# Kernel optimization log

Measured on AMD Instinct MI355X. Metric: run time of the kernel, lower is better.

## Reference

```python
import jax, jax.numpy as jnp
import numpy as np

B, T, N, H = 256, 128, 1024, 1024


def setup_inputs() -> dict:
    key = jax.random.key(0)
    ks = jax.random.split(key, 7)
    s = 0.05
    return {
        "input_data": jax.random.normal(ks[0], (B, T, N), jnp.float32),
        "W_ih": jax.random.normal(ks[1], (4 * H, N), jnp.float32) * s,
        "W_hh": jax.random.normal(ks[2], (4 * H, H), jnp.float32) * s,
        "b_ih": jax.random.normal(ks[3], (4 * H,), jnp.float32) * s,
        "b_hh": jax.random.normal(ks[4], (4 * H,), jnp.float32) * s,
        "attn_w": jax.random.normal(ks[5], (2 * H + T,), jnp.float32) * s,
        "attn_b": jax.random.normal(ks[6], (1,), jnp.float32) * s,
    }


def reference(input_data, W_ih, W_hh, b_ih, b_hh, attn_w, attn_b):
    # input_data: [B, T, N]; torch LSTM gate order i, f, g, o.
    Bsz, Tn, Nn = input_data.shape
    Hn = W_hh.shape[1]
    # Decompose the attn linear over the concat [h, c, x_hist]:
    # score = h @ w_h + c @ w_c + x_perm @ w_x + b  (exactly the original Linear)
    w_h, w_c, w_x = attn_w[:Hn], attn_w[Hn:2 * Hn], attn_w[2 * Hn:]
    x_perm = jnp.transpose(input_data, (0, 2, 1))            # [B, N, T]
    score_x = x_perm @ w_x + attn_b[0]                        # [B, N], constant over t

    def step(carry, x_t):
        h, c = carry                                          # [B, H] each
        score = (h @ w_h + c @ w_c)[:, None] + score_x        # [B, N]
        a = jax.nn.softmax(score, axis=1)                     # [B, N]
        w_in = a * x_t                                        # weighted input [B, N]
        gates = w_in @ W_ih.T + b_ih + h @ W_hh.T + b_hh      # [B, 4H]
        i, f, g, o = jnp.split(gates, 4, axis=1)
        c_new = jax.nn.sigmoid(f) * c + jax.nn.sigmoid(i) * jnp.tanh(g)
        h_new = jax.nn.sigmoid(o) * jnp.tanh(c_new)
        return (h_new, c_new), (w_in, h_new)

    h0 = jnp.zeros((Bsz, Hn), input_data.dtype)
    c0 = jnp.zeros((Bsz, Hn), input_data.dtype)
    xs = jnp.transpose(input_data, (1, 0, 2))                 # [T, B, N]
    _, (iw, ie) = jax.lax.scan(step, (h0, c0), xs)
    input_weighted = jnp.transpose(iw, (1, 0, 2))             # [B, T, N]
    input_encoded = jnp.transpose(ie, (1, 0, 2))              # [B, T, H]
    return input_weighted, input_encoded
```

## Files before the change

### kernel.cpp

```cpp
#include <hip/hip_runtime.h>
#include <hip/hip_bf16.h>

#define BB 256
#define TT 128
#define NN 1024
#define HH 1024
#define G4 4096

typedef __attribute__((ext_vector_type(4))) float f32x4;
typedef __attribute__((ext_vector_type(8))) short bf16x8;

__device__ __forceinline__ unsigned short f2bf(float f) {
    unsigned int u = __builtin_bit_cast(unsigned int, f);
    u += 0x7FFFu + ((u >> 16) & 1u);
    return (unsigned short)(u >> 16);
}
__device__ __forceinline__ float bf2f(unsigned short s) {
    unsigned int u = ((unsigned int)s) << 16;
    return __builtin_bit_cast(float, u);
}

__global__ __launch_bounds__(512) void k_attn(
    const float* __restrict__ x, const float* __restrict__ attn_w,
    const float* __restrict__ attn_b, float* __restrict__ out0,
    unsigned short* __restrict__ win_bf)
{
    const int b = blockIdx.x;
    const int tid = threadIdx.x;
    const float* xb = x + (size_t)b * (TT * NN);
    const float* wx = attn_w + 2 * HH;

    float s0 = 0.f, s1 = 0.f;
    for (int t = 0; t < TT; ++t) {
        float2 v = *(const float2*)(xb + (size_t)t * NN + tid * 2);
        float w = wx[t];
        s0 += v.x * w; s1 += v.y * w;
    }
    float ab = attn_b[0];
    s0 += ab; s1 += ab;

    __shared__ float red[8];
    const int wv = tid >> 6, ln = tid & 63;
    float m = fmaxf(s0, s1);
#pragma unroll
    for (int off = 32; off > 0; off >>= 1) m = fmaxf(m, __shfl_xor(m, off));
    if (ln == 0) red[wv] = m;
    __syncthreads();
    m = red[0];
#pragma unroll
    for (int i = 1; i < 8; ++i) m = fmaxf(m, red[i]);

    float e0 = expf(s0 - m), e1 = expf(s1 - m);
    float sum = e0 + e1;
#pragma unroll
    for (int off = 32; off > 0; off >>= 1) sum += __shfl_xor(sum, off);
    __syncthreads();
    if (ln == 0) red[wv] = sum;
    __syncthreads();
    sum = 0.f;
#pragma unroll
    for (int i = 0; i < 8; ++i) sum += red[i];
    const float inv = 1.0f / sum;
    const float a0 = e0 * inv, a1 = e1 * inv;

    float* o = out0 + (size_t)b * (TT * NN);
    unsigned short* wb = win_bf + (size_t)b * (TT * NN);
    for (int t = 0; t < TT; ++t) {
        float2 v = *(const float2*)(xb + (size_t)t * NN + tid * 2);
        float2 w; w.x = a0 * v.x; w.y = a1 * v.y;
        *(float2*)(o + (size_t)t * NN + tid * 2) = w;
        unsigned int pk = (unsigned int)f2bf(w.x) | ((unsigned int)f2bf(w.y) << 16);
        *(unsigned int*)(wb + (size_t)t * NN + tid * 2) = pk;
    }
}

__global__ __launch_bounds__(256) void k_prep_w(
    const float* __restrict__ Wih, const float* __restrict__ Whh,
    const float* __restrict__ bih, const float* __restrict__ bhh,
    unsigned short* __restrict__ WihP, unsigned short* __restrict__ WhhP,
    float* __restrict__ biasP)
{
    const int p = blockIdx.x;
    const int j = p >> 2, g = p & 3;
    const int r = g * HH + j;
    const int tid = threadIdx.x;
    {
        float4 v = *(const float4*)(Wih + (size_t)r * NN + tid * 4);
        ushort4 o;
        o.x = f2bf(v.x); o.y = f2bf(v.y); o.z = f2bf(v.z); o.w = f2bf(v.w);
        *(ushort4*)(WihP + (size_t)p * NN + tid * 4) = o;
    }
    {
        float4 v = *(const float4*)(Whh + (size_t)r * HH + tid * 4);
        ushort4 o;
        o.x = f2bf(v.x); o.y = f2bf(v.y); o.z = f2bf(v.z); o.w = f2bf(v.w);
        *(ushort4*)(WhhP + (size_t)p * HH + tid * 4) = o;
    }
    if (tid == 0) biasP[p] = bih[r] + bhh[r];
}

__global__ __launch_bounds__(256) void k_gemm_xp(
    const unsigned short* __restrict__ A,
    const unsigned short* __restrict__ Bm,
    unsigned short* __restrict__ C)
{
    __shared__ unsigned short lA[128 * 32];
    __shared__ unsigned short lB[128 * 32];

    const int bid = blockIdx.x;
    const int cpx = gridDim.x >> 3;
    const int swz = (bid & 7) * cpx + (bid >> 3);
    const int NTN = G4 / 128;
    const int tm = swz / NTN, tn = swz % NTN;

    const int tid = threadIdx.x;
    const int wv = tid >> 6, ln = tid & 63;
    const int wr = wv >> 1, wc = wv & 1;

    f32x4 acc[4][4] = {};

    const unsigned short* Ag = A + (size_t)tm * 128 * NN;
    const unsigned short* Bg = Bm + (size_t)tn * 128 * NN;
    const int srow = ln >> 2;
    const int sseg = ln & 3;

    for (int k0 = 0; k0 < NN; k0 += 32) {
        __syncthreads();
#pragma unroll
        for (int q = 0; q < 2; ++q) {
            const int row = wv * 32 + q * 16 + srow;
            __builtin_amdgcn_global_load_lds(
                (const __attribute__((address_space(1))) void*)(Ag + (size_t)row * NN + k0 + sseg * 8),
                (__attribute__((address_space(3))) void*)(&lA[(wv * 32 + q * 16) * 32]),
                16, 0, 0);
            __builtin_amdgcn_global_load_lds(
                (const __attribute__((address_space(1))) void*)(Bg + (size_t)row * NN + k0 + sseg * 8),
                (__attribute__((address_space(3))) void*)(&lB[(wv * 32 + q * 16) * 32]),
                16, 0, 0);
        }
        __syncthreads();

        const int rlo = ln & 15, khi = ln >> 4;
        bf16x8 af[4], bfr[4];
#pragma unroll
        for (int m = 0; m < 4; ++m)
            af[m] = *(const bf16x8*)&lA[(wr * 64 + m * 16 + rlo) * 32 + khi * 8];
#pragma unroll
        for (int n = 0; n < 4; ++n)
            bfr[n] = *(const bf16x8*)&lB[(wc * 64 + n * 16 + rlo) * 32 + khi * 8];
#pragma unroll
        for (int m = 0; m < 4; ++m)
#pragma unroll
            for (int n = 0; n < 4; ++n)
                acc[m][n] = __builtin_amdgcn_mfma_f32_16x16x32_bf16(af[m], bfr[n], acc[m][n], 0, 0, 0);
    }

    const int rlo = ln & 15, rhi = ln >> 4;
#pragma unroll
    for (int m = 0; m < 4; ++m)
#pragma unroll
        for (int n = 0; n < 4; ++n)
#pragma unroll
            for (int j = 0; j < 4; ++j) {
                const int row = tm * 128 + wr * 64 + m * 16 + rhi * 4 + j;
                const int col = tn * 128 + wc * 64 + n * 16 + rlo;
                C[(size_t)row * G4 + col] = f2bf(acc[m][n][j]);
            }
}

__global__ __launch_bounds__(512) void k_step3(
    const int t,
    const unsigned short* __restrict__ hbf,
    const unsigned short* __restrict__ WhhP,
    const unsigned short* __restrict__ Xp,
    const float* __restrict__ biasP,
    float* __restrict__ cbuf,
    unsigned short* __restrict__ hbf_out,
    float* __restrict__ out1)
{
    __shared__ unsigned short lA[3][64 * 128];
    __shared__ unsigned short lB[3][64 * 128];
    __shared__ unsigned short lXp[64 * 64];

    const int bid = blockIdx.x;
    const int ti = bid >> 6, tj = bid & 63;
    const int tid = threadIdx.x;
    const int wv = tid >> 6, ln = tid & 63;
    const int wr = wv >> 1, wc = wv & 1;
    const int rlo = ln & 15, khi = ln >> 4;

    {
        const size_t bg = (size_t)(ti * 64 + wv * 8 + (ln >> 3));
        __builtin_amdgcn_global_load_lds(
            (const __attribute__((address_space(1))) void*)((const char*)Xp + ((bg * TT + t) << 13) + tj * 128 + (ln & 7) * 16),
            (__attribute__((address_space(3))) void*)((char*)lXp + wv * 1024),
            16, 0, 0);
    }

    const char* Ab = (const char*)hbf + (size_t)(ti * 64) * 2048;
    const char* Bb = (const char*)WhhP + (size_t)(tj * 64) * 2048;

#define STAGE(buf_, c_) do { \
    _Pragma("unroll") \
    for (int q_ = 0; q_ < 2; ++q_) { \
        const int r_ = q_ * 32 + wv * 4 + (ln >> 4); \
        const int so_ = (((ln & 15) ^ (r_ & 7)) << 4); \
        __builtin_amdgcn_global_load_lds( \
            (const __attribute__((address_space(1))) void*)(Ab + (size_t)r_ * 2048 + (c_) * 256 + so_), \
            (__attribute__((address_space(3))) void*)((char*)&lA[buf_][0] + q_ * 8192 + wv * 1024), \
            16, 0, 0); \
        __builtin_amdgcn_global_load_lds( \
            (const __attribute__((address_space(1))) void*)(Bb + (size_t)r_ * 2048 + (c_) * 256 + so_), \
            (__attribute__((address_space(3))) void*)((char*)&lB[buf_][0] + q_ * 8192 + wv * 1024), \
            16, 0, 0); \
    } } while (0)

    STAGE(0, 0);
    STAGE(1, 1);
    STAGE(2, 2);

    float4 bias4[2];
#pragma unroll
    for (int n = 0; n < 2; ++n)
        bias4[n] = *(const float4*)&biasP[(tj * 16 + wc * 8 + n * 4 + ((ln & 15) >> 2)) * 4];

    f32x4 acc[2] = {};

#pragma unroll
    for (int c = 0; c < 8; ++c) {
        const int buf = c % 3;
        if (c < 6)       { asm volatile("s_waitcnt vmcnt(8)" ::: "memory"); }
        else if (c == 6) { asm volatile("s_waitcnt vmcnt(4)" ::: "memory"); }
        else             { asm volatile("s_waitcnt vmcnt(0)" ::: "memory"); }
        __builtin_amdgcn_s_barrier();

        bf16x8 af[4], bfr[4][2];
#pragma unroll
        for (int kk = 0; kk < 4; ++kk) {
            {
                const int row = wr * 16 + rlo;
                const int off = (kk * 64 + khi * 16) ^ ((row & 7) << 4);
                af[kk] = *(const bf16x8*)((const char*)&lA[buf][0] + row * 256 + off);
            }
#pragma unroll
            for (int n = 0; n < 2; ++n) {
                const int row = wc * 32 + n * 16 + rlo;
                const int off = (kk * 64 + khi * 16) ^ ((row & 7) << 4);
                bfr[kk][n] = *(const bf16x8*)((const char*)&lB[buf][0] + row * 256 + off);
            }
        }
        asm volatile("s_waitcnt lgkmcnt(0)" ::: "memory");
        __builtin_amdgcn_sched_barrier(0);
        __builtin_amdgcn_s_barrier();
        if (c < 5) STAGE((c + 3) % 3, c + 3);
#pragma unroll
        for (int kk = 0; kk < 4; ++kk)
#pragma unroll
            for (int n = 0; n < 2; ++n)
                acc[n] = __builtin_amdgcn_mfma_f32_16x16x32_bf16(af[kk], bfr[kk][n], acc[n], 0, 0, 0);
    }
#undef STAGE

#pragma unroll
    for (int n = 0; n < 2; ++n) {
        f32x4 v = acc[n], u, w;
#pragma unroll
        for (int k = 0; k < 4; ++k) {
            float s = __shfl_xor(v[k ^ 1], 1);
            u[k] = ((k & 1) == (ln & 1)) ? v[k] : s;
        }
#pragma unroll
        for (int k = 0; k < 4; ++k) {
            float s = __shfl_xor(u[k ^ 2], 2);
            w[k] = (((k >> 1) & 1) == ((ln >> 1) & 1)) ? u[k] : s;
        }
        const int r_loc = wr * 16 + ((ln >> 4) << 2) + (ln & 3);
        const int u_loc = wc * 8 + n * 4 + ((ln & 15) >> 2);
        const ushort4 xp4 = *(const ushort4*)((const char*)lXp + r_loc * 128 + u_loc * 8);
        const float gi = w[0] + bf2f(xp4.x) + bias4[n].x;
        const float gf = w[1] + bf2f(xp4.y) + bias4[n].y;
        const float gg = w[2] + bf2f(xp4.z) + bias4[n].z;
        const float go = w[3] + bf2f(xp4.w) + bias4[n].w;
        const float i_ = 1.f / (1.f + expf(-gi));
        const float f_ = 1.f / (1.f + expf(-gf));
        const float g_ = tanhf(gg);
        const float o_ = 1.f / (1.f + expf(-go));
        const int bg = ti * 64 + r_loc;
        const int ug = tj * 16 + u_loc;
        const float cprev = cbuf[(size_t)bg * HH + ug];
        const float cc = f_ * cprev + i_ * g_;
        cbuf[(size_t)bg * HH + ug] = cc;
        const float h_ = o_ * tanhf(cc);
        out1[(size_t)bg * (TT * HH) + (size_t)t * HH + ug] = h_;
        hbf_out[(size_t)bg * HH + ug] = f2bf(h_);
    }
}

__global__ __launch_bounds__(256) void k_zero(float4* __restrict__ p)
{
    p[blockIdx.x * 256 + threadIdx.x] = make_float4(0.f, 0.f, 0.f, 0.f);
}

extern "C" void kernel_launch(void* const* d_in, const int* in_sizes, int n_in,
                              void* d_out, int out_size, void* d_ws, size_t ws_size,
                              hipStream_t stream)
{
    const float* x      = (const float*)d_in[0];
    const float* Wih    = (const float*)d_in[1];
    const float* Whh    = (const float*)d_in[2];
    const float* bih    = (const float*)d_in[3];
    const float* bhh    = (const float*)d_in[4];
    const float* attn_w = (const float*)d_in[5];
    const float* attn_b = (const float*)d_in[6];

    float* out0 = (float*)d_out;
    float* out1 = (float*)d_out + (size_t)BB * TT * NN;

    char* w = (char*)d_ws;
    unsigned short* WihP  = (unsigned short*)(w);
    unsigned short* WhhP  = (unsigned short*)(w + 8388608);
    float*          biasP = (float*)(w + 16777216);
    unsigned short* winbf = (unsigned short*)(w + 16793600);
    unsigned short* Xp    = (unsigned short*)(w + 83902464);
    unsigned short* hbf0  = (unsigned short*)(w + 352337920);
    unsigned short* hbf1  = (unsigned short*)(w + 352862208);
    float*          cbuf  = (float*)(w + 353386496);

    k_attn<<<BB, 512, 0, stream>>>(x, attn_w, attn_b, out0, winbf);
    k_prep_w<<<G4, 256, 0, stream>>>(Wih, Whh, bih, bhh, WihP, WhhP, biasP);
    k_gemm_xp<<<(BB * TT / 128) * (G4 / 128), 256, 0, stream>>>(winbf, WihP, Xp);
    k_zero<<<512, 256, 0, stream>>>((float4*)hbf0);

    for (int t = 0; t < TT; ++t) {
        const unsigned short* hin = (t & 1) ? hbf1 : hbf0;
        unsigned short* hout      = (t & 1) ? hbf0 : hbf1;
        k_step3<<<256, 512, 0, stream>>>(t, hin, WhhP, Xp, biasP, cbuf, hout, out1);
    }
}
```

Before: 1.717 ms.

## Replace per-timestep launches with persistent cooperative LSTM recurrence kernel

Adds a persistent cooperative kernel that runs all 128 timesteps in one launch. Each block keeps its slice of W_hh resident in LDS for the whole sequence and keeps the cell state in registers. Blocks sharing a batch tile synchronise through per-tile atomic counters in global memory instead of kernel boundaries. This removes per-step launch overhead and repeated W_hh reloads, at the cost of spin-wait latency, reliance on every block being co-resident, and reuse of the cbuf region as counters. The old per-step launch loop is kept as a fallback if the cooperative launch fails.

Result: slower. 2.731 ms (+59.0%).

```diff
diff --git a/kernel.cpp b/kernel.cpp
--- a/kernel.cpp
+++ b/kernel.cpp
@@ -166,6 +166,154 @@
                 const int col = tn * 128 + wc * 64 + n * 16 + rlo;
                 C[(size_t)row * G4 + col] = f2bf(acc[m][n][j]);
             }
+}
+
+__global__ __launch_bounds__(512, 1) void k_recur2(
+    const unsigned short* __restrict__ WhhP,
+    const unsigned short* __restrict__ Xp,
+    const float* __restrict__ biasP,
+    unsigned short* __restrict__ h0,
+    unsigned short* __restrict__ h1,
+    unsigned int* __restrict__ ctr,
+    float* __restrict__ out1)
+{
+    __shared__ unsigned short lB[64 * 1024];
+    __shared__ unsigned short lA[3][64 * 64];
+
+    const int bid = blockIdx.x;
+    const int ti = bid >> 6, tj = bid & 63;
+    const int tid = threadIdx.x;
+    const int wv = tid >> 6, ln = tid & 63;
+    const int wr = wv >> 1, wc = wv & 1;
+    const int rlo = ln & 15, khi = ln >> 4;
+
+    {
+        const char* base = (const char*)WhhP + (size_t)(tj * 64) * 2048;
+#pragma unroll
+        for (int q = 0; q < 16; ++q) {
+            const int i = wv * 16 + q;
+            const int r = i >> 1, half = i & 1;
+            const int lbo = (half * 1024 + ln * 16) ^ ((r & 7) << 4);
+            __builtin_amdgcn_global_load_lds(
+                (const __attribute__((address_space(1))) void*)(base + (size_t)r * 2048 + lbo),
+                (__attribute__((address_space(3))) void*)((char*)lB + i * 1024),
+                16, 0, 0);
+        }
+    }
+
+    float4 bias4[2];
+#pragma unroll
+    for (int n = 0; n < 2; ++n)
+        bias4[n] = *(const float4*)&biasP[(tj * 16 + wc * 8 + n * 4 + ((ln & 15) >> 2)) * 4];
+
+    const int r_loc = wr * 16 + ((ln >> 4) << 2) + (ln & 3);
+    const int u_loc0 = wc * 8 + ((ln & 15) >> 2);
+    const int bg = ti * 64 + r_loc;
+    unsigned int* myctr = &ctr[ti * 64];
+
+    float c_reg[2] = {0.f, 0.f};
+
+#define STAGE_H(buf_, c_) do { \
+    const int r_ = wv * 8 + (ln >> 3); \
+    const int so_ = ((ln & 7) << 4) ^ ((r_ & 7) << 4); \
+    __builtin_amdgcn_global_load_lds( \
+        (const __attribute__((address_space(1))) void*)(Ab + (size_t)r_ * 2048 + (c_) * 128 + so_), \
+        (__attribute__((address_space(3))) void*)((char*)&lA[buf_][0] + wv * 1024), \
+        16, 0, 0); \
+} while (0)
+
+    for (int t = 0; t < TT; ++t) {
+        const unsigned short* hR = (t & 1) ? h1 : h0;
+        unsigned short* hW = (t & 1) ? h0 : h1;
+
+        ushort4 xp4[2];
+#pragma unroll
+        for (int n = 0; n < 2; ++n)
+            xp4[n] = *(const ushort4*)((const char*)Xp +
+                        ((size_t)bg * TT + t) * 8192 + tj * 128 + (u_loc0 + n * 4) * 8);
+
+        f32x4 acc[2] = {};
+
+        if (t > 0) {
+            if (tid == 0) {
+                const unsigned int want = 64u * (unsigned int)t;
+                while (__hip_atomic_load(myctr, __ATOMIC_RELAXED, __HIP_MEMORY_SCOPE_AGENT) < want)
+                    __builtin_amdgcn_s_sleep(2);
+                (void)__hip_atomic_load(myctr, __ATOMIC_ACQUIRE, __HIP_MEMORY_SCOPE_AGENT);
+            }
+            __syncthreads();
+
+            const char* Ab = (const char*)hR + (size_t)(ti * 64) * 2048;
+            STAGE_H(0, 0);
+            STAGE_H(1, 1);
+#pragma unroll
+            for (int c = 0; c < 16; ++c) {
+                const int buf = c % 3;
+                if (c < 15) { asm volatile("s_waitcnt vmcnt(1)" ::: "memory"); }
+                else        { asm volatile("s_waitcnt vmcnt(0)" ::: "memory"); }
+                __builtin_amdgcn_s_barrier();
+                if (c < 14) STAGE_H((c + 2) % 3, c + 2);
+
+                bf16x8 af[2], bfr[2][2];
+#pragma unroll
+                for (int kk = 0; kk < 2; ++kk) {
+                    {
+                        const int row = wr * 16 + rlo;
+                        const int off = (kk * 64 + khi * 16) ^ ((row & 7) << 4);
+                        af[kk] = *(const bf16x8*)((const char*)&lA[buf][0] + row * 128 + off);
+                    }
+#pragma unroll
+                    for (int n = 0; n < 2; ++n) {
+                        const int row = wc * 32 + n * 16 + rlo;
+                        const int off = (c * 128 + kk * 64 + khi * 16) ^ ((row & 7) << 4);
+                        bfr[kk][n] = *(const bf16x8*)((const char*)lB + row * 2048 + off);
+                    }
+                }
+                asm volatile("s_waitcnt lgkmcnt(0)" ::: "memory");
+                __builtin_amdgcn_sched_barrier(0);
+#pragma unroll
+                for (int kk = 0; kk < 2; ++kk)
+#pragma unroll
+                    for (int n = 0; n < 2; ++n)
+                        acc[n] = __builtin_amdgcn_mfma_f32_16x16x32_bf16(af[kk], bfr[kk][n], acc[n], 0, 0, 0);
+            }
+        }
+
+#pragma unroll
+        for (int n = 0; n < 2; ++n) {
+            f32x4 v = acc[n], u, w;
+#pragma unroll
+            for (int k = 0; k < 4; ++k) {
+                float s = __shfl_xor(v[k ^ 1], 1);
+                u[k] = ((k & 1) == (ln & 1)) ? v[k] : s;
+            }
+#pragma unroll
+            for (int k = 0; k < 4; ++k) {
+                float s = __shfl_xor(u[k ^ 2], 2);
+                w[k] = (((k >> 1) & 1) == ((ln >> 1) & 1)) ? u[k] : s;
+            }
+            const float gi = w[0] + bf2f(xp4[n].x) + bias4[n].x;
+            const float gf = w[1] + bf2f(xp4[n].y) + bias4[n].y;
+            const float gg = w[2] + bf2f(xp4[n].z) + bias4[n].z;
+            const float go = w[3] + bf2f(xp4[n].w) + bias4[n].w;
+            const float i_ = 1.f / (1.f + expf(-gi));
+            const float f_ = 1.f / (1.f + expf(-gf));
+            const float g_ = tanhf(gg);
+            const float o_ = 1.f / (1.f + expf(-go));
+            const float cc = f_ * c_reg[n] + i_ * g_;
+            c_reg[n] = cc;
+            const float h_ = o_ * tanhf(cc);
+            const int ug = tj * 16 + u_loc0 + n * 4;
+            __builtin_nontemporal_store(h_, &out1[(size_t)bg * (TT * HH) + (size_t)t * HH + ug]);
+            hW[(size_t)bg * HH + ug] = f2bf(h_);
+        }
+
+        asm volatile("s_waitcnt vmcnt(0)" ::: "memory");
+        __syncthreads();
+        if (tid == 0)
+            __hip_atomic_fetch_add(myctr, 1u, __ATOMIC_RELEASE, __HIP_MEMORY_SCOPE_AGENT);
+    }
+#undef STAGE_H
 }
 
 __global__ __launch_bounds__(512) void k_step3(
@@ -331,9 +479,24 @@
     k_gemm_xp<<<(BB * TT / 128) * (G4 / 128), 256, 0, stream>>>(winbf, WihP, Xp);
     k_zero<<<512, 256, 0, stream>>>((float4*)hbf0);
 
-    for (int t = 0; t < TT; ++t) {
-        const unsigned short* hin = (t & 1) ? hbf1 : hbf0;
-        unsigned short* hout      = (t & 1) ? hbf0 : hbf1;
-        k_step3<<<256, 512, 0, stream>>>(t, hin, WhhP, Xp, biasP, cbuf, hout, out1);
-    }
-}
+    {
+        const unsigned short* WhhP_c = WhhP;
+        const unsigned short* Xp_c = Xp;
+        const float* biasP_c = biasP;
+        unsigned short* h0_c = hbf0;
+        unsigned short* h1_c = hbf1;
+        unsigned int* ctr_c = (unsigned int*)cbuf;
+        float* out1_c = out1;
+        void* args[] = { (void*)&WhhP_c, (void*)&Xp_c, (void*)&biasP_c,
+                         (void*)&h0_c, (void*)&h1_c, (void*)&ctr_c, (void*)&out1_c };
+        hipError_t err = hipLaunchCooperativeKernel((void*)k_recur2, dim3(256), dim3(512),
+                                                    args, 0, stream);
+        if (err != hipSuccess) {
+            for (int t = 0; t < TT; ++t) {
+                const unsigned short* hin = (t & 1) ? hbf1 : hbf0;
+                unsigned short* hout      = (t & 1) ? hbf0 : hbf1;
+                k_step3<<<256, 512, 0, stream>>>(t, hin, WhhP, Xp, biasP, cbuf, hout, out1);
+            }
+        }
+    }
+}
```

## Restructure LSTM step kernel: full-K LDS weight tile, direct-register h loads

Applied to the files above, without the earlier changes.

The per-step recurrent GEMM kernel is rewritten to stage the whole 64x1024 W_hh tile into LDS in two halves through registers, replacing the triple-buffered global_load_lds pipeline over K chunks. The h operand is now read straight from global memory into registers instead of through LDS. The Xp slice, previous cell state and bias are prefetched into registers at kernel start, which removes most per-chunk barriers. The cost is 128KB of LDS per block and heavy register use, with launch_bounds(512,2) added as an occupancy hint.

New measurement: 2.232 ms. +30.0%, slower.

```diff
diff --git a/kernel.cpp b/kernel.cpp
--- a/kernel.cpp
+++ b/kernel.cpp
@@ -168,7 +168,7 @@
             }
 }
 
-__global__ __launch_bounds__(512) void k_step3(
+__global__ __launch_bounds__(512, 2) void k_step4(
     const int t,
     const unsigned short* __restrict__ hbf,
     const unsigned short* __restrict__ WhhP,
@@ -178,9 +178,7 @@
     unsigned short* __restrict__ hbf_out,
     float* __restrict__ out1)
 {
-    __shared__ unsigned short lA[3][64 * 128];
-    __shared__ unsigned short lB[3][64 * 128];
-    __shared__ unsigned short lXp[64 * 64];
+    __shared__ unsigned short lB[64 * 1024];
 
     const int bid = blockIdx.x;
     const int ti = bid >> 6, tj = bid & 63;
@@ -188,78 +186,95 @@
     const int wv = tid >> 6, ln = tid & 63;
     const int wr = wv >> 1, wc = wv & 1;
     const int rlo = ln & 15, khi = ln >> 4;
-
-    {
-        const size_t bg = (size_t)(ti * 64 + wv * 8 + (ln >> 3));
-        __builtin_amdgcn_global_load_lds(
-            (const __attribute__((address_space(1))) void*)((const char*)Xp + ((bg * TT + t) << 13) + tj * 128 + (ln & 7) * 16),
-            (__attribute__((address_space(3))) void*)((char*)lXp + wv * 1024),
-            16, 0, 0);
-    }
+    const int khi16 = khi * 16;
 
     const char* Ab = (const char*)hbf + (size_t)(ti * 64) * 2048;
     const char* Bb = (const char*)WhhP + (size_t)(tj * 64) * 2048;
 
-#define STAGE(buf_, c_) do { \
-    _Pragma("unroll") \
-    for (int q_ = 0; q_ < 2; ++q_) { \
-        const int r_ = q_ * 32 + wv * 4 + (ln >> 4); \
-        const int so_ = (((ln & 15) ^ (r_ & 7)) << 4); \
-        __builtin_amdgcn_global_load_lds( \
-            (const __attribute__((address_space(1))) void*)(Ab + (size_t)r_ * 2048 + (c_) * 256 + so_), \
-            (__attribute__((address_space(3))) void*)((char*)&lA[buf_][0] + q_ * 8192 + wv * 1024), \
-            16, 0, 0); \
-        __builtin_amdgcn_global_load_lds( \
-            (const __attribute__((address_space(1))) void*)(Bb + (size_t)r_ * 2048 + (c_) * 256 + so_), \
-            (__attribute__((address_space(3))) void*)((char*)&lB[buf_][0] + q_ * 8192 + wv * 1024), \
-            16, 0, 0); \
-    } } while (0)
-
-    STAGE(0, 0);
-    STAGE(1, 1);
-    STAGE(2, 2);
-
+    const int r_loc = wr * 16 + ((ln >> 4) << 2) + (ln & 3);
+    const int u_loc0 = wc * 8 + ((ln & 15) >> 2);
+    const int bg = ti * 64 + r_loc;
+
+    ushort4 xp4[2];
+    float cp[2];
     float4 bias4[2];
 #pragma unroll
-    for (int n = 0; n < 2; ++n)
-        bias4[n] = *(const float4*)&biasP[(tj * 16 + wc * 8 + n * 4 + ((ln & 15) >> 2)) * 4];
+    for (int n = 0; n < 2; ++n) {
+        xp4[n] = *(const ushort4*)((const char*)Xp +
+                    ((size_t)bg * TT + t) * 8192 + tj * 128 + (u_loc0 + n * 4) * 8);
+        cp[n] = cbuf[(size_t)bg * HH + tj * 16 + u_loc0 + n * 4];
+        bias4[n] = *(const float4*)&biasP[(tj * 16 + u_loc0 + n * 4) * 4];
+    }
+
+    const int srow = tid >> 3;
+    const int sseg = tid & 7;
+    const int sswz = (srow & 7) << 4;
+
+    bf16x8 bh1[8];
+#pragma unroll
+    for (int j = 0; j < 8; ++j)
+        bh1[j] = *(const bf16x8*)(Bb + (size_t)srow * 2048 + (sseg + j * 8) * 16);
+
+    const char* abase = Ab + (size_t)(wr * 16 + rlo) * 2048 + khi16;
+#define LOADA(c) \
+    const bf16x8 a0_##c = *(const bf16x8*)(abase + (c) * 128); \
+    const bf16x8 a1_##c = *(const bf16x8*)(abase + (c) * 128 + 64);
+    LOADA(0) LOADA(1) LOADA(2) LOADA(3) LOADA(4) LOADA(5) LOADA(6) LOADA(7)
+
+    bf16x8 bh2[8];
+#pragma unroll
+    for (int j = 0; j < 8; ++j)
+        bh2[j] = *(const bf16x8*)(Bb + (size_t)srow * 2048 + 1024 + (sseg + j * 8) * 16);
+
+    char* lw = (char*)lB + (size_t)srow * 2048;
+#pragma unroll
+    for (int j = 0; j < 8; ++j)
+        *(bf16x8*)(lw + (((sseg + j * 8) * 16) ^ sswz)) = bh1[j];
+
+    asm volatile("s_waitcnt lgkmcnt(0)" ::: "memory");
+    __builtin_amdgcn_sched_barrier(0);
+    __builtin_amdgcn_s_barrier();
+
+    const int brow0 = wc * 32 + rlo;
+    const int bswz = (brow0 & 7) << 4;
+    const char* lb0 = (const char*)lB + (size_t)brow0 * 2048;
+    const char* lb1 = lb0 + 16 * 2048;
+    const int okk0 = khi16 ^ bswz;
+    const int okk1 = (64 + khi16) ^ bswz;
 
     f32x4 acc[2] = {};
 
-#pragma unroll
-    for (int c = 0; c < 8; ++c) {
-        const int buf = c % 3;
-        if (c < 6)       { asm volatile("s_waitcnt vmcnt(8)" ::: "memory"); }
-        else if (c == 6) { asm volatile("s_waitcnt vmcnt(4)" ::: "memory"); }
-        else             { asm volatile("s_waitcnt vmcnt(0)" ::: "memory"); }
-        __builtin_amdgcn_s_barrier();
-
-        bf16x8 af[4], bfr[4][2];
-#pragma unroll
-        for (int kk = 0; kk < 4; ++kk) {
-            {
-                const int row = wr * 16 + rlo;
-                const int off = (kk * 64 + khi * 16) ^ ((row & 7) << 4);
-                af[kk] = *(const bf16x8*)((const char*)&lA[buf][0] + row * 256 + off);
-            }
-#pragma unroll
-            for (int n = 0; n < 2; ++n) {
-                const int row = wc * 32 + n * 16 + rlo;
-                const int off = (kk * 64 + khi * 16) ^ ((row & 7) << 4);
-                bfr[kk][n] = *(const bf16x8*)((const char*)&lB[buf][0] + row * 256 + off);
-            }
-        }
-        asm volatile("s_waitcnt lgkmcnt(0)" ::: "memory");
-        __builtin_amdgcn_sched_barrier(0);
-        __builtin_amdgcn_s_barrier();
-        if (c < 5) STAGE((c + 3) % 3, c + 3);
-#pragma unroll
-        for (int kk = 0; kk < 4; ++kk)
-#pragma unroll
-            for (int n = 0; n < 2; ++n)
-                acc[n] = __builtin_amdgcn_mfma_f32_16x16x32_bf16(af[kk], bfr[kk][n], acc[n], 0, 0, 0);
-    }
-#undef STAGE
+#define CHUNK(c) do { \
+    const bf16x8 b00 = *(const bf16x8*)(lb0 + (c) * 128 + okk0); \
+    const bf16x8 b01 = *(const bf16x8*)(lb0 + (c) * 128 + okk1); \
+    const bf16x8 b10 = *(const bf16x8*)(lb1 + (c) * 128 + okk0); \
+    const bf16x8 b11 = *(const bf16x8*)(lb1 + (c) * 128 + okk1); \
+    acc[0] = __builtin_amdgcn_mfma_f32_16x16x32_bf16(a0_##c, b00, acc[0], 0, 0, 0); \
+    acc[1] = __builtin_amdgcn_mfma_f32_16x16x32_bf16(a0_##c, b10, acc[1], 0, 0, 0); \
+    acc[0] = __builtin_amdgcn_mfma_f32_16x16x32_bf16(a1_##c, b01, acc[0], 0, 0, 0); \
+    acc[1] = __builtin_amdgcn_mfma_f32_16x16x32_bf16(a1_##c, b11, acc[1], 0, 0, 0); \
+} while (0)
+
+    CHUNK(0); CHUNK(1); CHUNK(2);
+
+#pragma unroll
+    for (int j = 0; j < 8; ++j)
+        *(bf16x8*)(lw + 1024 + (((sseg + j * 8) * 16) ^ sswz)) = bh2[j];
+
+    CHUNK(3); CHUNK(4);
+    LOADA(8) LOADA(9) LOADA(10) LOADA(11)
+    CHUNK(5); CHUNK(6);
+    LOADA(12) LOADA(13) LOADA(14) LOADA(15)
+    CHUNK(7);
+
+    asm volatile("s_waitcnt lgkmcnt(0)" ::: "memory");
+    __builtin_amdgcn_sched_barrier(0);
+    __builtin_amdgcn_s_barrier();
+
+    CHUNK(8); CHUNK(9); CHUNK(10); CHUNK(11);
+    CHUNK(12); CHUNK(13); CHUNK(14); CHUNK(15);
+#undef CHUNK
+#undef LOADA
 
 #pragma unroll
     for (int n = 0; n < 2; ++n) {
@@ -274,23 +289,18 @@
             float s = __shfl_xor(u[k ^ 2], 2);
             w[k] = (((k >> 1) & 1) == ((ln >> 1) & 1)) ? u[k] : s;
         }
-        const int r_loc = wr * 16 + ((ln >> 4) << 2) + (ln & 3);
-        const int u_loc = wc * 8 + n * 4 + ((ln & 15) >> 2);
-        const ushort4 xp4 = *(const ushort4*)((const char*)lXp + r_loc * 128 + u_loc * 8);
-        const float gi = w[0] + bf2f(xp4.x) + bias4[n].x;
-        const float gf = w[1] + bf2f(xp4.y) + bias4[n].y;
-        const float gg = w[2] + bf2f(xp4.z) + bias4[n].z;
-        const float go = w[3] + bf2f(xp4.w) + bias4[n].w;
+        const float gi = w[0] + bf2f(xp4[n].x) + bias4[n].x;
+        const float gf = w[1] + bf2f(xp4[n].y) + bias4[n].y;
+        const float gg = w[2] + bf2f(xp4[n].z) + bias4[n].z;
+        const float go = w[3] + bf2f(xp4[n].w) + bias4[n].w;
         const float i_ = 1.f / (1.f + expf(-gi));
         const float f_ = 1.f / (1.f + expf(-gf));
         const float g_ = tanhf(gg);
         const float o_ = 1.f / (1.f + expf(-go));
-        const int bg = ti * 64 + r_loc;
-        const int ug = tj * 16 + u_loc;
-        const float cprev = cbuf[(size_t)bg * HH + ug];
-        const float cc = f_ * cprev + i_ * g_;
+        const float cc = f_ * cp[n] + i_ * g_;
+        const float h_ = o_ * tanhf(cc);
+        const int ug = tj * 16 + u_loc0 + n * 4;
         cbuf[(size_t)bg * HH + ug] = cc;
-        const float h_ = o_ * tanhf(cc);
         out1[(size_t)bg * (TT * HH) + (size_t)t * HH + ug] = h_;
         hbf_out[(size_t)bg * HH + ug] = f2bf(h_);
     }
@@ -334,6 +344,6 @@
     for (int t = 0; t < TT; ++t) {
         const unsigned short* hin = (t & 1) ? hbf1 : hbf0;
         unsigned short* hout      = (t & 1) ? hbf0 : hbf1;
-        k_step3<<<256, 512, 0, stream>>>(t, hin, WhhP, Xp, biasP, cbuf, hout, out1);
-    }
-}
+        k_step4<<<256, 512, 0, stream>>>(t, hin, WhhP, Xp, biasP, cbuf, hout, out1);
+    }
+}
```

## Rewrite input-projection GEMM with 256x256 tiles and triple-buffered async LDS pipeline

Applied to the files above, without the earlier changes.

Replaces the 128x128-tile input projection GEMM with a 512-thread kernel using 256x256 tiles, a 64-wide K chunk and a three-stage LDS ring filled by global_load_lds. Explicit vmcnt waits and barriers let the next loads overlap with the MFMA work, and s_setprio raises priority during the MFMA section. The aim is more reuse per loaded byte and hidden global latency in the big precompute GEMM. In exchange it uses much more LDS and registers, which limits occupancy to one block per CU, and it depends on hand-tuned waitcnt counts being correct.

Measured after the change: 1.832 ms. +6.7%, slower.

```diff
diff --git a/kernel.cpp b/kernel.cpp
--- a/kernel.cpp
+++ b/kernel.cpp
@@ -99,71 +99,85 @@
     if (tid == 0) biasP[p] = bih[r] + bhh[r];
 }
 
-__global__ __launch_bounds__(256) void k_gemm_xp(
+__global__ __launch_bounds__(512, 1) void k_gemm_xp2(
     const unsigned short* __restrict__ A,
     const unsigned short* __restrict__ Bm,
     unsigned short* __restrict__ C)
 {
-    __shared__ unsigned short lA[128 * 32];
-    __shared__ unsigned short lB[128 * 32];
+    __shared__ unsigned short lA[3][4][256][8];
+    __shared__ unsigned short lB[3][4][256][8];
 
     const int bid = blockIdx.x;
     const int cpx = gridDim.x >> 3;
     const int swz = (bid & 7) * cpx + (bid >> 3);
-    const int NTN = G4 / 128;
+    const int NTN = G4 / 256;
     const int tm = swz / NTN, tn = swz % NTN;
 
     const int tid = threadIdx.x;
     const int wv = tid >> 6, ln = tid & 63;
-    const int wr = wv >> 1, wc = wv & 1;
-
-    f32x4 acc[4][4] = {};
-
-    const unsigned short* Ag = A + (size_t)tm * 128 * NN;
-    const unsigned short* Bg = Bm + (size_t)tn * 128 * NN;
-    const int srow = ln >> 2;
-    const int sseg = ln & 3;
-
-    for (int k0 = 0; k0 < NN; k0 += 32) {
-        __syncthreads();
-#pragma unroll
-        for (int q = 0; q < 2; ++q) {
-            const int row = wv * 32 + q * 16 + srow;
-            __builtin_amdgcn_global_load_lds(
-                (const __attribute__((address_space(1))) void*)(Ag + (size_t)row * NN + k0 + sseg * 8),
-                (__attribute__((address_space(3))) void*)(&lA[(wv * 32 + q * 16) * 32]),
-                16, 0, 0);
-            __builtin_amdgcn_global_load_lds(
-                (const __attribute__((address_space(1))) void*)(Bg + (size_t)row * NN + k0 + sseg * 8),
-                (__attribute__((address_space(3))) void*)(&lB[(wv * 32 + q * 16) * 32]),
-                16, 0, 0);
-        }
-        __syncthreads();
-
-        const int rlo = ln & 15, khi = ln >> 4;
-        bf16x8 af[4], bfr[4];
-#pragma unroll
-        for (int m = 0; m < 4; ++m)
-            af[m] = *(const bf16x8*)&lA[(wr * 64 + m * 16 + rlo) * 32 + khi * 8];
+    const int wm = wv >> 2, wn = wv & 3;
+    const int rlo = ln & 15, khi = ln >> 4;
+
+    const char* Ag = (const char*)A + (size_t)(tm * 256) * 2048;
+    const char* Bg = (const char*)Bm + (size_t)(tn * 256) * 2048;
+
+#define STAGE(buf_, c_) do { \
+    _Pragma("unroll") \
+    for (int j_ = 0; j_ < 2; ++j_) { \
+        const int seg_ = (wv * 2 + j_) * 64 + ln; \
+        const int khi_ = seg_ >> 8, row_ = seg_ & 255; \
+        __builtin_amdgcn_global_load_lds( \
+            (const __attribute__((address_space(1))) void*)(Ag + (size_t)row_ * 2048 + (c_) * 64 + khi_ * 16), \
+            (__attribute__((address_space(3))) void*)((char*)&lA[buf_][0][0][0] + (wv * 2 + j_) * 1024), \
+            16, 0, 0); \
+        __builtin_amdgcn_global_load_lds( \
+            (const __attribute__((address_space(1))) void*)(Bg + (size_t)row_ * 2048 + (c_) * 64 + khi_ * 16), \
+            (__attribute__((address_space(3))) void*)((char*)&lB[buf_][0][0][0] + (wv * 2 + j_) * 1024), \
+            16, 0, 0); \
+    } } while (0)
+
+    STAGE(0, 0); STAGE(1, 1); STAGE(2, 2);
+
+    f32x4 acc[8][4] = {};
+
+    for (int c = 0; c < 32; ++c) {
+        const int buf = c % 3;
+        if (c < 30)       { asm volatile("s_waitcnt vmcnt(8)" ::: "memory"); }
+        else if (c == 30) { asm volatile("s_waitcnt vmcnt(4)" ::: "memory"); }
+        else              { asm volatile("s_waitcnt vmcnt(0)" ::: "memory"); }
+        __builtin_amdgcn_s_barrier();
+
+        bf16x8 af[8], bfr[4];
+#pragma unroll
+        for (int m = 0; m < 8; ++m)
+            af[m] = *(const bf16x8*)&lA[buf][khi][wm * 128 + m * 16 + rlo][0];
 #pragma unroll
         for (int n = 0; n < 4; ++n)
-            bfr[n] = *(const bf16x8*)&lB[(wc * 64 + n * 16 + rlo) * 32 + khi * 8];
-#pragma unroll
-        for (int m = 0; m < 4; ++m)
+            bfr[n] = *(const bf16x8*)&lB[buf][khi][wn * 64 + n * 16 + rlo][0];
+        asm volatile("s_waitcnt lgkmcnt(0)" ::: "memory");
+        __builtin_amdgcn_sched_barrier(0);
+        __builtin_amdgcn_s_barrier();
+        if (c < 29) STAGE(buf, c + 3);
+
+        __builtin_amdgcn_s_setprio(1);
+#pragma unroll
+        for (int m = 0; m < 8; ++m)
 #pragma unroll
             for (int n = 0; n < 4; ++n)
                 acc[m][n] = __builtin_amdgcn_mfma_f32_16x16x32_bf16(af[m], bfr[n], acc[m][n], 0, 0, 0);
-    }
-
-    const int rlo = ln & 15, rhi = ln >> 4;
-#pragma unroll
-    for (int m = 0; m < 4; ++m)
+        __builtin_amdgcn_s_setprio(0);
+    }
+#undef STAGE
+
+    const int rhi = ln >> 4;
+#pragma unroll
+    for (int m = 0; m < 8; ++m)
 #pragma unroll
         for (int n = 0; n < 4; ++n)
 #pragma unroll
             for (int j = 0; j < 4; ++j) {
-                const int row = tm * 128 + wr * 64 + m * 16 + rhi * 4 + j;
-                const int col = tn * 128 + wc * 64 + n * 16 + rlo;
+                const int row = tm * 256 + wm * 128 + m * 16 + rhi * 4 + j;
+                const int col = tn * 256 + wn * 64 + n * 16 + rlo;
                 C[(size_t)row * G4 + col] = f2bf(acc[m][n][j]);
             }
 }
@@ -328,7 +342,7 @@
 
     k_attn<<<BB, 512, 0, stream>>>(x, attn_w, attn_b, out0, winbf);
     k_prep_w<<<G4, 256, 0, stream>>>(Wih, Whh, bih, bhh, WihP, WhhP, biasP);
-    k_gemm_xp<<<(BB * TT / 128) * (G4 / 128), 256, 0, stream>>>(winbf, WihP, Xp);
+    k_gemm_xp2<<<(BB * TT / 256) * (G4 / 256), 512, 0, stream>>>(winbf, WihP, Xp);
     k_zero<<<512, 256, 0, stream>>>((float4*)hbf0);
 
     for (int t = 0; t < TT; ++t) {
```
